# Performance work log

Hardware: AMD Instinct MI355X
Metric: run time of the kernel (lower is better)

## Reference

```python
import jax, jax.numpy as jnp
import numpy as np

V, E, T_MAX, H, L = 20000, 384, 512, 8, 8
D = E // H  # head size 48
FF = 4 * E


def setup_inputs() -> dict:
    key = jax.random.key(0)
    ks = jax.random.split(key, 24)
    B, T = 16, 512
    s = 0.02
    return {
        "index": jax.random.randint(ks[0], (B, T), 0, V, dtype=jnp.int64),
        "targets": jax.random.randint(ks[1], (B, T), 0, V, dtype=jnp.int64),
        "tok_emb": s * jax.random.normal(ks[2], (V, E), jnp.float32),
        "pos_emb": s * jax.random.normal(ks[3], (T_MAX, E), jnp.float32),
        "Wq": s * jax.random.normal(ks[4], (L, E, H, D), jnp.float32),
        "bq": jnp.zeros((L, H, D), jnp.float32),
        "Wk": s * jax.random.normal(ks[5], (L, E, H, D), jnp.float32),
        "bk": jnp.zeros((L, H, D), jnp.float32),
        "Wv": s * jax.random.normal(ks[6], (L, E, H, D), jnp.float32),
        "bv": jnp.zeros((L, H, D), jnp.float32),
        "Wo": s * jax.random.normal(ks[7], (L, E, E), jnp.float32),
        "bo": jnp.zeros((L, E), jnp.float32),
        "ln1_g": jnp.ones((L, E), jnp.float32),
        "ln1_b": jnp.zeros((L, E), jnp.float32),
        "ln2_g": jnp.ones((L, E), jnp.float32),
        "ln2_b": jnp.zeros((L, E), jnp.float32),
        "W1": s * jax.random.normal(ks[8], (L, E, FF), jnp.float32),
        "b1": jnp.zeros((L, FF), jnp.float32),
        "W2": s * jax.random.normal(ks[9], (L, FF, E), jnp.float32),
        "b2": jnp.zeros((L, E), jnp.float32),
        "lnf_g": jnp.ones((E,), jnp.float32),
        "lnf_b": jnp.zeros((E,), jnp.float32),
        "lm_b": jnp.zeros((V,), jnp.float32),
    }


def layernorm(x, g, b, eps=1e-5):
    mu = jnp.mean(x, axis=-1, keepdims=True)
    var = jnp.var(x, axis=-1, keepdims=True)
    return (x - mu) * jax.lax.rsqrt(var + eps) * g + b


def reference(index, targets, tok_emb, pos_emb, Wq, bq, Wk, bk, Wv, bv, Wo, bo,
              ln1_g, ln1_b, ln2_g, ln2_b, W1, b1, W2, b2, lnf_g, lnf_b, lm_b):
    B, T = index.shape
    x = tok_emb[index] + pos_emb[:T]  # [B,T,E]
    causal = jnp.tril(jnp.ones((T, T), bool))
    scale = D ** -0.5
    for l in range(L):
        h = layernorm(x, ln1_g[l], ln1_b[l])
        q = jnp.einsum('bte,ehd->bthd', h, Wq[l]) + bq[l]
        k = jnp.einsum('bte,ehd->bthd', h, Wk[l]) + bk[l]
        v = jnp.einsum('bte,ehd->bthd', h, Wv[l]) + bv[l]
        scores = jnp.einsum('bqhd,bkhd->bhqk', q, k) * scale
        scores = jnp.where(causal, scores, -jnp.inf)
        w = jax.nn.softmax(scores, axis=-1)
        attn = jnp.einsum('bhqk,bkhd->bqhd', w, v).reshape(B, T, E)
        x = x + attn @ Wo[l] + bo[l]
        h2 = layernorm(x, ln2_g[l], ln2_b[l])
        ff = jax.nn.gelu(h2 @ W1[l] + b1[l], approximate=False) @ W2[l] + b2[l]
        x = x + ff
    x = layernorm(x, lnf_g, lnf_b)
    logits = x @ tok_emb.T + lm_b  # tied weights
    logits = logits.reshape(B * T, V)
    logp = jax.nn.log_softmax(logits, axis=-1)
    loss = -jnp.mean(jnp.take_along_axis(logp, targets.reshape(-1, 1), axis=-1))
    return logits, loss
```

## Files before the change

### kernel.cpp

```cpp
#include <hip/hip_runtime.h>
#include <hip/hip_bf16.h>
#include <math.h>

#define M_ROWS 8192
#define E_DIM 384
#define FF_DIM 1536
#define V_DIM 20000
#define VPAD 20096
#define N_LAYER 8
#define QK_SCALE 0.14433756729740643f
#define PSTRIDE 320

typedef __bf16 bf16x8 __attribute__((ext_vector_type(8)));
typedef short  s16x8  __attribute__((ext_vector_type(8)));
typedef float  f32x4  __attribute__((ext_vector_type(4)));
typedef __hip_bfloat16 bf16_t;

__device__ __forceinline__ void gl2lds16(const void* g, void* l) {
    __builtin_amdgcn_global_load_lds((const __attribute__((address_space(1))) void*)g,
                                     (__attribute__((address_space(3))) void*)l, 16, 0, 0);
}

__global__ __launch_bounds__(256) void tconv_kernel(
    const float* __restrict__ in, bf16_t* __restrict__ out,
    int K, int N, int outRows, int rowoff)
{
    __shared__ float tile[32][33];
    const int n0 = blockIdx.x * 32, k0 = blockIdx.y * 32;
    const float* ip = in + (size_t)blockIdx.z * K * N;
    bf16_t* op = out + (size_t)blockIdx.z * outRows * K;
    const int tx = threadIdx.x & 31, ty = threadIdx.x >> 5;
#pragma unroll
    for (int i = 0; i < 32; i += 8)
        tile[ty + i][tx] = ip[(size_t)(k0 + ty + i) * N + n0 + tx];
    __syncthreads();
#pragma unroll
    for (int i = 0; i < 32; i += 8)
        op[(size_t)(rowoff + n0 + ty + i) * K + k0 + tx] = __float2bfloat16(tile[tx][ty + i]);
}

__global__ __launch_bounds__(256) void tokconv_kernel(
    const float* __restrict__ tok, bf16_t* __restrict__ out)
{
    const size_t total = (size_t)VPAD * E_DIM;
    for (size_t i = blockIdx.x * 256ull + threadIdx.x; i < total; i += gridDim.x * 256ull) {
        int row = (int)(i / E_DIM);
        int col = (int)(i - (size_t)row * E_DIM);
        float v = (row < V_DIM) ? tok[(size_t)row * E_DIM + col] : 0.f;
        out[i] = __float2bfloat16(v);
    }
}

__global__ __launch_bounds__(256) void bqkv_kernel(
    const float* __restrict__ bq, const float* __restrict__ bk,
    const float* __restrict__ bv, float* __restrict__ o)
{
    int i = blockIdx.x * 256 + threadIdx.x;
    if (i < N_LAYER * 1152) {
        int l = i / 1152, c = i - l * 1152;
        float v = (c < 384) ? bq[l * 384 + c] : (c < 768) ? bk[l * 384 + c - 384] : bv[l * 384 + c - 768];
        o[i] = v;
    }
}

__global__ __launch_bounds__(256) void embed_kernel(
    const int* __restrict__ idx, const float* __restrict__ tok,
    const float* __restrict__ pos, float* __restrict__ x)
{
    int row = blockIdx.x * 4 + (threadIdx.x >> 6);
    int lane = threadIdx.x & 63;
    int t = row & 511;
    int id = idx[row];
    const float* tr = tok + (size_t)id * E_DIM;
    const float* pr = pos + (size_t)t * E_DIM;
    float* xr = x + (size_t)row * E_DIM;
#pragma unroll
    for (int i = 0; i < 6; i++) { int c = lane + i * 64; xr[c] = tr[c] + pr[c]; }
}

__global__ __launch_bounds__(256) void ln_kernel(
    const float* __restrict__ x, const float* __restrict__ g,
    const float* __restrict__ b, bf16_t* __restrict__ out)
{
    int row = blockIdx.x * 4 + (threadIdx.x >> 6);
    int lane = threadIdx.x & 63;
    const float* xr = x + (size_t)row * E_DIM;
    float vals[6];
    float s = 0.f;
#pragma unroll
    for (int i = 0; i < 6; i++) { vals[i] = xr[lane + i * 64]; s += vals[i]; }
#pragma unroll
    for (int off = 1; off < 64; off <<= 1) s += __shfl_xor(s, off);
    float mu = s * (1.f / E_DIM);
    float sq = 0.f;
#pragma unroll
    for (int i = 0; i < 6; i++) { float d = vals[i] - mu; sq += d * d; }
#pragma unroll
    for (int off = 1; off < 64; off <<= 1) sq += __shfl_xor(sq, off);
    float rstd = rsqrtf(sq * (1.f / E_DIM) + 1e-5f);
    bf16_t* orow = out + (size_t)row * E_DIM;
#pragma unroll
    for (int i = 0; i < 6; i++) {
        int c = lane + i * 64;
        orow[c] = __float2bfloat16((vals[i] - mu) * rstd * g[c] + b[c]);
    }
}

template <int MODE, int MREP>
__global__ __launch_bounds__(256) void gemm_kernel(
    const bf16_t* __restrict__ A, const bf16_t* __restrict__ Bt,
    const float* __restrict__ bias, void* __restrict__ Cv, void* __restrict__ C2,
    int Ncols, int K)
{
    constexpr int BMR = MREP * 32;
    __shared__ __align__(16) short smem[8192];
    const int t = threadIdx.x;
    const int w = t >> 6, lane = t & 63;
    const int wm = w >> 1, wn = w & 1;
    const int bm = (MODE == 3 ? blockIdx.x : blockIdx.y) * BMR;
    const int bn = (MODE == 3 ? blockIdx.y : blockIdx.x) * 128;

    f32x4 acc[MREP][4];
#pragma unroll
    for (int m = 0; m < MREP; m++)
#pragma unroll
        for (int n = 0; n < 4; n++)
            acc[m][n] = (f32x4){0.f, 0.f, 0.f, 0.f};

    const int lg = lane >> 4;
    const int ll = lane & 15;

    for (int kt = 0; kt < K; kt += 32) {
        __syncthreads();
#pragma unroll
        for (int i = 0; i < MREP / 2; i++) {
            int li = i * 256 + t;
            int g = li >> (MREP == 4 ? 7 : 6);
            int row = li & (BMR - 1);
            gl2lds16(A + (size_t)(bm + row) * K + kt + g * 8,
                     smem + (size_t)(i * 256 + w * 64) * 8);
        }
#pragma unroll
        for (int i = 0; i < 2; i++) {
            gl2lds16(Bt + (size_t)(bn + ((i * 256 + t) & 127)) * K + kt + ((i * 256 + t) >> 7) * 8,
                     smem + 4096 + (size_t)(i * 256 + w * 64) * 8);
        }
        asm volatile("s_waitcnt vmcnt(0)" ::: "memory");
        __syncthreads();

        bf16x8 af[MREP], bfr[4];
#pragma unroll
        for (int m = 0; m < MREP; m++)
            af[m] = __builtin_bit_cast(bf16x8,
                *(const s16x8*)&smem[(lg * BMR + wm * (BMR / 2) + m * 16 + ll) * 8]);
#pragma unroll
        for (int n = 0; n < 4; n++)
            bfr[n] = __builtin_bit_cast(bf16x8,
                *(const s16x8*)&smem[4096 + (lg * 128 + wn * 64 + n * 16 + ll) * 8]);
#pragma unroll
        for (int m = 0; m < MREP; m++)
#pragma unroll
            for (int n = 0; n < 4; n++)
                acc[m][n] = __builtin_amdgcn_mfma_f32_16x16x32_bf16(af[m], bfr[n], acc[m][n], 0, 0, 0);
    }

    const int r0 = bm + wm * (BMR / 2) + (lane >> 4) * 4;
    const int c0 = bn + wn * 64 + (lane & 15);

    if (MODE == 4) {
        bf16_t* qkvb = (bf16_t*)Cv;
        bf16_t* vtb  = (bf16_t*)C2;
        const int rgn = bn / 384;
#pragma unroll
        for (int n = 0; n < 4; n++) {
            int col = c0 + n * 16;
            float bv = bias[col];
            if (rgn < 2) {
                const float sc = (rgn == 0) ? QK_SCALE : 1.f;
#pragma unroll
                for (int m = 0; m < MREP; m++) {
#pragma unroll
                    for (int j = 0; j < 4; j++) {
                        int row = r0 + m * 16 + j;
                        qkvb[(size_t)row * 1152 + col] = __float2bfloat16((acc[m][n][j] + bv) * sc);
                    }
                }
            } else {
                int cc = col - 768;
                int hh = cc / 48, dd = cc - hh * 48;
#pragma unroll
                for (int m = 0; m < MREP; m++) {
                    int row0 = r0 + m * 16;
                    int bb = row0 >> 9, tt = row0 & 511;
                    ushort4 pk;
                    pk.x = __builtin_bit_cast(unsigned short, __float2bfloat16(acc[m][n][0] + bv));
                    pk.y = __builtin_bit_cast(unsigned short, __float2bfloat16(acc[m][n][1] + bv));
                    pk.z = __builtin_bit_cast(unsigned short, __float2bfloat16(acc[m][n][2] + bv));
                    pk.w = __builtin_bit_cast(unsigned short, __float2bfloat16(acc[m][n][3] + bv));
                    *(ushort4*)&vtb[((size_t)(bb * 8 + hh) * 48 + dd) * 512 + tt] = pk;
                }
            }
        }
        return;
    }

    if (MODE == 3) {
        float* C = (float*)Cv;
        float* pbuf = (float*)C2;
        const int ptile = blockIdx.y * 2 + wn;
        float bvv[4];
#pragma unroll
        for (int n = 0; n < 4; n++) {
            int col = c0 + n * 16;
            bvv[n] = (col < Ncols) ? bias[col] : 0.f;
        }
#pragma unroll
        for (int m = 0; m < MREP; m++) {
#pragma unroll
            for (int j = 0; j < 4; j++) {
                int row = r0 + m * 16 + j;
                float se = 0.f;
#pragma unroll
                for (int n = 0; n < 4; n++) {
                    int col = c0 + n * 16;
                    if (col < Ncols) {
                        float v = acc[m][n][j] + bvv[n];
                        C[(size_t)row * Ncols + col] = v;
                        se += __expf(v);
                    }
                }
                se += __shfl_xor(se, 1);
                se += __shfl_xor(se, 2);
                se += __shfl_xor(se, 4);
                se += __shfl_xor(se, 8);
                if (ll == 0) pbuf[(size_t)row * PSTRIDE + ptile] = se;
            }
        }
        return;
    }

#pragma unroll
    for (int n = 0; n < 4; n++) {
        int col = c0 + n * 16;
        float bv = bias[col];
#pragma unroll
        for (int m = 0; m < MREP; m++) {
#pragma unroll
            for (int j = 0; j < 4; j++) {
                int row = r0 + m * 16 + j;
                float v = acc[m][n][j] + bv;
                if (MODE == 1) {
                    float* C = (float*)Cv;
                    C[(size_t)row * Ncols + col] += v;
                } else {
                    v = 0.5f * v * (1.f + erff(v * 0.70710678118654752f));
                    ((bf16_t*)Cv)[(size_t)row * Ncols + col] = __float2bfloat16(v);
                }
            }
        }
    }
}

__global__ __launch_bounds__(256) void attn_kernel(
    const bf16_t* __restrict__ qkvb, const bf16_t* __restrict__ vt,
    bf16_t* __restrict__ o)
{
    const int qt = blockIdx.x, bh = blockIdx.y;
    const int b = bh >> 3, h = bh & 7;
    __shared__ unsigned short psm[4608];
    const int tid = threadIdx.x;
    const int w = tid >> 6, lane = tid & 63;
    const int ll = lane & 15, g = lane >> 4;
    const int q0 = qt * 64;
    const int q_abs = q0 + ll * 4 + w;

    const bf16_t* qrow = qkvb + (size_t)(b * 512 + q_abs) * 1152 + h * 48;
    bf16x8 qf0 = __builtin_bit_cast(bf16x8, *(const s16x8*)(qrow + g * 8));
    bf16x8 qf1 = {};
    if (g < 2) qf1 = __builtin_bit_cast(bf16x8, *(const s16x8*)(qrow + 32 + g * 8));

    f32x4 oacc[3];
#pragma unroll
    for (int df = 0; df < 3; df++) oacc[df] = (f32x4){0.f, 0.f, 0.f, 0.f};
    float mrun = -1e30f, ssum = 0.f;

    const bf16_t* kb0 = qkvb + (size_t)b * 512 * 1152 + 384 + h * 48;
    const bf16_t* vb0 = vt + (size_t)bh * 48 * 512;
    const int ntiles = 2 * (qt + 1);

    for (int kt = 0; kt < ntiles; kt++) {
        const int kbase = kt * 32;
        f32x4 sfr[2];
#pragma unroll
        for (int f = 0; f < 2; f++) {
            const bf16_t* krow = kb0 + (size_t)(kbase + f * 16 + ll) * 1152;
            bf16x8 k0 = __builtin_bit_cast(bf16x8, *(const s16x8*)(krow + g * 8));
            bf16x8 k1 = {};
            if (g < 2) k1 = __builtin_bit_cast(bf16x8, *(const s16x8*)(krow + 32 + g * 8));
            f32x4 z = {0.f, 0.f, 0.f, 0.f};
            z = __builtin_amdgcn_mfma_f32_16x16x32_bf16(k0, qf0, z, 0, 0, 0);
            z = __builtin_amdgcn_mfma_f32_16x16x32_bf16(k1, qf1, z, 0, 0, 0);
            sfr[f] = z;
        }
        bf16x8 vf[3];
#pragma unroll
        for (int df = 0; df < 3; df++)
            vf[df] = __builtin_bit_cast(bf16x8,
                *(const s16x8*)(vb0 + (size_t)(df * 16 + ll) * 512 + kbase + g * 8));

        float p[8];
        float tmax = -1e30f;
#pragma unroll
        for (int f = 0; f < 2; f++)
#pragma unroll
            for (int j = 0; j < 4; j++) {
                int key = kbase + f * 16 + g * 4 + j;
                float sv = sfr[f][j];
                sv = (key > q_abs) ? -1e30f : sv;
                p[f * 4 + j] = sv;
                tmax = fmaxf(tmax, sv);
            }
        tmax = fmaxf(tmax, __shfl_xor(tmax, 16));
        tmax = fmaxf(tmax, __shfl_xor(tmax, 32));
        float mnew = fmaxf(mrun, tmax);
        float corr = __expf(mrun - mnew);
        float psum = 0.f;
#pragma unroll
        for (int i = 0; i < 8; i++) { p[i] = __expf(p[i] - mnew); psum += p[i]; }
        psum += __shfl_xor(psum, 16);
        psum += __shfl_xor(psum, 32);
        ssum = ssum * corr + psum;
        mrun = mnew;
#pragma unroll
        for (int df = 0; df < 3; df++)
#pragma unroll
            for (int j = 0; j < 4; j++) oacc[df][j] *= corr;

        const int pbase = (w * 2 + (kt & 1)) * 576;
#pragma unroll
        for (int f = 0; f < 2; f++)
#pragma unroll
            for (int j = 0; j < 4; j++)
                psm[pbase + (f * 16 + g * 4 + j) * 18 + ll] =
                    __builtin_bit_cast(unsigned short, __float2bfloat16(p[f * 4 + j]));
        s16x8 pr;
#pragma unroll
        for (int i = 0; i < 8; i++)
            pr[i] = (short)psm[pbase + (g * 8 + i) * 18 + ll];
        bf16x8 pf = __builtin_bit_cast(bf16x8, pr);
#pragma unroll
        for (int df = 0; df < 3; df++)
            oacc[df] = __builtin_amdgcn_mfma_f32_16x16x32_bf16(vf[df], pf, oacc[df], 0, 0, 0);
    }

    float inv = 1.f / ssum;
    bf16_t* orow = o + (size_t)(b * 512 + q_abs) * 384 + h * 48;
#pragma unroll
    for (int df = 0; df < 3; df++) {
        ushort4 pk;
        pk.x = __builtin_bit_cast(unsigned short, __float2bfloat16(oacc[df][0] * inv));
        pk.y = __builtin_bit_cast(unsigned short, __float2bfloat16(oacc[df][1] * inv));
        pk.z = __builtin_bit_cast(unsigned short, __float2bfloat16(oacc[df][2] * inv));
        pk.w = __builtin_bit_cast(unsigned short, __float2bfloat16(oacc[df][3] * inv));
        *(ushort4*)&orow[df * 16 + g * 4] = pk;
    }
}

__global__ __launch_bounds__(256) void loss_row2_kernel(
    const float* __restrict__ pbuf, const float* __restrict__ logits,
    const int* __restrict__ targets, float* __restrict__ rowloss)
{
    int row = blockIdx.x * 4 + (threadIdx.x >> 6);
    int lane = threadIdx.x & 63;
    const float* pr = pbuf + (size_t)row * PSTRIDE;
    float s = 0.f;
    for (int i = lane; i < 314; i += 64) s += pr[i];
#pragma unroll
    for (int off = 1; off < 64; off <<= 1) s += __shfl_xor(s, off);
    if (lane == 0) {
        int tgt = targets[row];
        rowloss[row] = logf(s) - logits[(size_t)row * V_DIM + tgt];
    }
}

__global__ __launch_bounds__(256) void loss_reduce_kernel(
    const float* __restrict__ rowloss, float* __restrict__ out)
{
    int t = threadIdx.x;
    __shared__ float red[4];
    float s = 0.f;
    for (int i = t; i < M_ROWS; i += 256) s += rowloss[i];
#pragma unroll
    for (int off = 1; off < 64; off <<= 1) s += __shfl_xor(s, off);
    if ((t & 63) == 0) red[t >> 6] = s;
    __syncthreads();
    if (t == 0) out[0] = (red[0] + red[1] + red[2] + red[3]) * (1.f / M_ROWS);
}

extern "C" void kernel_launch(void* const* d_in, const int* in_sizes, int n_in,
                              void* d_out, int out_size, void* d_ws, size_t ws_size,
                              hipStream_t stream)
{
    const int*   index   = (const int*)d_in[0];
    const int*   targets = (const int*)d_in[1];
    const float* tok_emb = (const float*)d_in[2];
    const float* pos_emb = (const float*)d_in[3];
    const float* Wq = (const float*)d_in[4];
    const float* bq = (const float*)d_in[5];
    const float* Wk = (const float*)d_in[6];
    const float* bk = (const float*)d_in[7];
    const float* Wv = (const float*)d_in[8];
    const float* bv = (const float*)d_in[9];
    const float* Wo = (const float*)d_in[10];
    const float* bo = (const float*)d_in[11];
    const float* ln1_g = (const float*)d_in[12];
    const float* ln1_b = (const float*)d_in[13];
    const float* ln2_g = (const float*)d_in[14];
    const float* ln2_b = (const float*)d_in[15];
    const float* W1 = (const float*)d_in[16];
    const float* b1 = (const float*)d_in[17];
    const float* W2 = (const float*)d_in[18];
    const float* b2 = (const float*)d_in[19];
    const float* lnf_g = (const float*)d_in[20];
    const float* lnf_b = (const float*)d_in[21];
    const float* lm_b  = (const float*)d_in[22];

    float* out = (float*)d_out;
    char* wsb = (char*)d_ws;

    float*  x     = (float*)(wsb + 0);
    bf16_t* hbuf  = (bf16_t*)(wsb + 12582912);
    bf16_t* obuf  = (bf16_t*)(wsb + 18874368);
    bf16_t* qkvb  = (bf16_t*)(wsb + 25165824);
    bf16_t* vtb   = (bf16_t*)(wsb + 44040192);
    bf16_t* ffmid = (bf16_t*)(wsb + 18874368);
    bf16_t* tokb  = (bf16_t*)(wsb + 50331648);
    bf16_t* qkvw  = (bf16_t*)(wsb + 65765376);
    bf16_t* wo_t  = (bf16_t*)(wsb + 72843264);
    bf16_t* w1_t  = (bf16_t*)(wsb + 75202560);
    bf16_t* w2_t  = (bf16_t*)(wsb + 84639744);
    float*  bqkv  = (float*)(wsb + 94076928);
    float*  rowloss = (float*)(wsb + 94113792);
    float*  pbuf  = (float*)(wsb + 94146560);

    tokconv_kernel<<<2048, 256, 0, stream>>>(tok_emb, tokb);
    tconv_kernel<<<dim3(12, 12, 8), 256, 0, stream>>>(Wq, qkvw, 384, 384, 1152, 0);
    tconv_kernel<<<dim3(12, 12, 8), 256, 0, stream>>>(Wk, qkvw, 384, 384, 1152, 384);
    tconv_kernel<<<dim3(12, 12, 8), 256, 0, stream>>>(Wv, qkvw, 384, 384, 1152, 768);
    tconv_kernel<<<dim3(12, 12, 8), 256, 0, stream>>>(Wo, wo_t, 384, 384, 384, 0);
    tconv_kernel<<<dim3(48, 12, 8), 256, 0, stream>>>(W1, w1_t, 384, 1536, 1536, 0);
    tconv_kernel<<<dim3(12, 48, 8), 256, 0, stream>>>(W2, w2_t, 1536, 384, 384, 0);
    bqkv_kernel<<<36, 256, 0, stream>>>(bq, bk, bv, bqkv);

    embed_kernel<<<2048, 256, 0, stream>>>(index, tok_emb, pos_emb, x);

    for (int l = 0; l < N_LAYER; l++) {
        ln_kernel<<<2048, 256, 0, stream>>>(x, ln1_g + l * E_DIM, ln1_b + l * E_DIM, hbuf);
        gemm_kernel<4, 4><<<dim3(9, 64), 256, 0, stream>>>(
            hbuf, qkvw + (size_t)l * 1152 * 384, bqkv + l * 1152, qkvb, vtb, 1152, 384);
        attn_kernel<<<dim3(8, 128), 256, 0, stream>>>(qkvb, vtb, obuf);
        gemm_kernel<1, 2><<<dim3(3, 128), 256, 0, stream>>>(
            obuf, wo_t + (size_t)l * 384 * 384, bo + l * E_DIM, x, nullptr, 384, 384);
        ln_kernel<<<2048, 256, 0, stream>>>(x, ln2_g + l * E_DIM, ln2_b + l * E_DIM, hbuf);
        gemm_kernel<2, 4><<<dim3(12, 64), 256, 0, stream>>>(
            hbuf, w1_t + (size_t)l * 1536 * 384, b1 + l * FF_DIM, ffmid, nullptr, 1536, 384);
        gemm_kernel<1, 2><<<dim3(3, 128), 256, 0, stream>>>(
            ffmid, w2_t + (size_t)l * 384 * 1536, b2 + l * E_DIM, x, nullptr, 384, 1536);
    }

    ln_kernel<<<2048, 256, 0, stream>>>(x, lnf_g, lnf_b, hbuf);
    gemm_kernel<3, 4><<<dim3(64, 157), 256, 0, stream>>>(
        hbuf, tokb, lm_b, out, pbuf, V_DIM, 384);

    loss_row2_kernel<<<2048, 256, 0, stream>>>(pbuf, out, targets, rowloss);
    loss_reduce_kernel<<<1, 256, 0, stream>>>(rowloss, out + (size_t)M_ROWS * V_DIM);
}
```

Baseline: 2.021 ms.

## Double-buffer GEMM LDS tiles to overlap global loads with MFMA

The GEMM kernel's shared-memory staging becomes a two-buffer ping-pong. Each iteration issues the next K-tile's global-to-LDS loads, then waits only for the current tile with a partial vmcnt before the MFMAs, so load latency overlaps compute. This doubles LDS use to 32 KB per block, which may lower occupancy. Correctness depends on vmcnt(NLD) matching the number of loads issued per stage.

```diff
diff --git a/kernel.cpp b/kernel.cpp
--- a/kernel.cpp
+++ b/kernel.cpp
@@ -113,7 +113,8 @@
     int Ncols, int K)
 {
     constexpr int BMR = MREP * 32;
-    __shared__ __align__(16) short smem[8192];
+    constexpr int NLD = MREP / 2 + 2;
+    __shared__ __align__(16) short smem[16384];
     const int t = threadIdx.x;
     const int w = t >> 6, lane = t & 63;
     const int wm = w >> 1, wn = w & 1;
@@ -129,39 +130,55 @@
 
     const int lg = lane >> 4;
     const int ll = lane & 15;
-
-    for (int kt = 0; kt < K; kt += 32) {
-        __syncthreads();
+    const int nt = K / 32;
+
+    auto stagef = [&](int kt, int buf) {
+        short* sA = smem + buf * 8192;
+        short* sB = sA + 4096;
 #pragma unroll
         for (int i = 0; i < MREP / 2; i++) {
             int li = i * 256 + t;
             int g = li >> (MREP == 4 ? 7 : 6);
             int row = li & (BMR - 1);
             gl2lds16(A + (size_t)(bm + row) * K + kt + g * 8,
-                     smem + (size_t)(i * 256 + w * 64) * 8);
+                     sA + (size_t)(i * 256 + w * 64) * 8);
         }
 #pragma unroll
         for (int i = 0; i < 2; i++) {
-            gl2lds16(Bt + (size_t)(bn + ((i * 256 + t) & 127)) * K + kt + ((i * 256 + t) >> 7) * 8,
-                     smem + 4096 + (size_t)(i * 256 + w * 64) * 8);
-        }
-        asm volatile("s_waitcnt vmcnt(0)" ::: "memory");
-        __syncthreads();
-
+            int li = i * 256 + t;
+            gl2lds16(Bt + (size_t)(bn + (li & 127)) * K + kt + (li >> 7) * 8,
+                     sB + (size_t)(i * 256 + w * 64) * 8);
+        }
+    };
+
+    stagef(0, 0);
+    for (int tt = 0; tt < nt; ++tt) {
+        const int buf = tt & 1;
+        if (tt + 1 < nt) {
+            stagef((tt + 1) * 32, buf ^ 1);
+            asm volatile("s_waitcnt vmcnt(%0)" :: "n"(NLD) : "memory");
+        } else {
+            asm volatile("s_waitcnt vmcnt(0)" ::: "memory");
+        }
+        __builtin_amdgcn_s_barrier();
+
+        const short* sA = smem + buf * 8192;
+        const short* sB = sA + 4096;
         bf16x8 af[MREP], bfr[4];
 #pragma unroll
         for (int m = 0; m < MREP; m++)
             af[m] = __builtin_bit_cast(bf16x8,
-                *(const s16x8*)&smem[(lg * BMR + wm * (BMR / 2) + m * 16 + ll) * 8]);
+                *(const s16x8*)&sA[(lg * BMR + wm * (BMR / 2) + m * 16 + ll) * 8]);
 #pragma unroll
         for (int n = 0; n < 4; n++)
             bfr[n] = __builtin_bit_cast(bf16x8,
-                *(const s16x8*)&smem[4096 + (lg * 128 + wn * 64 + n * 16 + ll) * 8]);
+                *(const s16x8*)&sB[(lg * 128 + wn * 64 + n * 16 + ll) * 8]);
 #pragma unroll
         for (int m = 0; m < MREP; m++)
 #pragma unroll
             for (int n = 0; n < 4; n++)
                 acc[m][n] = __builtin_amdgcn_mfma_f32_16x16x32_bf16(af[m], bfr[n], acc[m][n], 0, 0, 0);
+        __builtin_amdgcn_s_barrier();
     }
 
     const int r0 = bm + wm * (BMR / 2) + (lane >> 4) * 4;
@@ -191,13 +208,13 @@
 #pragma unroll
                 for (int m = 0; m < MREP; m++) {
                     int row0 = r0 + m * 16;
-                    int bb = row0 >> 9, tt = row0 & 511;
+                    int bb = row0 >> 9, tt2 = row0 & 511;
                     ushort4 pk;
                     pk.x = __builtin_bit_cast(unsigned short, __float2bfloat16(acc[m][n][0] + bv));
                     pk.y = __builtin_bit_cast(unsigned short, __float2bfloat16(acc[m][n][1] + bv));
                     pk.z = __builtin_bit_cast(unsigned short, __float2bfloat16(acc[m][n][2] + bv));
                     pk.w = __builtin_bit_cast(unsigned short, __float2bfloat16(acc[m][n][3] + bv));
-                    *(ushort4*)&vtb[((size_t)(bb * 8 + hh) * 48 + dd) * 512 + tt] = pk;
+                    *(ushort4*)&vtb[((size_t)(bb * 8 + hh) * 48 + dd) * 512 + tt2] = pk;
                 }
             }
         }
```

After: 2.036 ms. No clear change (+0.8%).

## Swap MFMA operands so GEMM epilogues write vectorized row-contiguous outputs

Applied to the files above, without the earlier changes.

Adds a SWAP template flag that swaps the A/B operands of the MFMA, so each lane holds four consecutive output columns of one row. The epilogues for QK projection, Wo/W2 residual add, GELU FFN and LM head can then use float4 bias loads and packed 4-wide stores instead of scalar strided stores. The QKV GEMM is split into a swapped Q/K launch and a separate non-swapped V launch that keeps the transposed V layout. This targets uncoalesced epilogue store traffic, notably the large logits write, at the cost of one extra kernel launch per layer and re-reading hbuf for V.

```diff
diff --git a/kernel.cpp b/kernel.cpp
--- a/kernel.cpp
+++ b/kernel.cpp
@@ -20,6 +20,9 @@
     __builtin_amdgcn_global_load_lds((const __attribute__((address_space(1))) void*)g,
                                      (__attribute__((address_space(3))) void*)l, 16, 0, 0);
 }
+__device__ __forceinline__ unsigned short bf16bits(float v) {
+    return __builtin_bit_cast(unsigned short, __float2bfloat16(v));
+}
 
 __global__ __launch_bounds__(256) void tconv_kernel(
     const float* __restrict__ in, bf16_t* __restrict__ out,
@@ -106,7 +109,7 @@
     }
 }
 
-template <int MODE, int MREP>
+template <int MODE, int MREP, bool SWAP>
 __global__ __launch_bounds__(256) void gemm_kernel(
     const bf16_t* __restrict__ A, const bf16_t* __restrict__ Bt,
     const float* __restrict__ bias, void* __restrict__ Cv, void* __restrict__ C2,
@@ -142,7 +145,8 @@
         }
 #pragma unroll
         for (int i = 0; i < 2; i++) {
-            gl2lds16(Bt + (size_t)(bn + ((i * 256 + t) & 127)) * K + kt + ((i * 256 + t) >> 7) * 8,
+            int li = i * 256 + t;
+            gl2lds16(Bt + (size_t)(bn + (li & 127)) * K + kt + (li >> 7) * 8,
                      smem + 4096 + (size_t)(i * 256 + w * 64) * 8);
         }
         asm volatile("s_waitcnt vmcnt(0)" ::: "memory");
@@ -160,102 +164,133 @@
 #pragma unroll
         for (int m = 0; m < MREP; m++)
 #pragma unroll
-            for (int n = 0; n < 4; n++)
-                acc[m][n] = __builtin_amdgcn_mfma_f32_16x16x32_bf16(af[m], bfr[n], acc[m][n], 0, 0, 0);
-    }
-
-    const int r0 = bm + wm * (BMR / 2) + (lane >> 4) * 4;
-    const int c0 = bn + wn * 64 + (lane & 15);
-
-    if (MODE == 4) {
-        bf16_t* qkvb = (bf16_t*)Cv;
-        bf16_t* vtb  = (bf16_t*)C2;
-        const int rgn = bn / 384;
-#pragma unroll
-        for (int n = 0; n < 4; n++) {
-            int col = c0 + n * 16;
-            float bv = bias[col];
-            if (rgn < 2) {
-                const float sc = (rgn == 0) ? QK_SCALE : 1.f;
+            for (int n = 0; n < 4; n++) {
+                if (SWAP)
+                    acc[m][n] = __builtin_amdgcn_mfma_f32_16x16x32_bf16(bfr[n], af[m], acc[m][n], 0, 0, 0);
+                else
+                    acc[m][n] = __builtin_amdgcn_mfma_f32_16x16x32_bf16(af[m], bfr[n], acc[m][n], 0, 0, 0);
+            }
+    }
+
+    if constexpr (SWAP) {
+        const int rowm0 = bm + wm * (BMR / 2) + ll;
+        const int coln0 = bn + wn * 64 + lg * 4;
+
+        if constexpr (MODE == 4) {
+            bf16_t* qkvb = (bf16_t*)Cv;
+            const float sc = (bn >= 384) ? 1.f : QK_SCALE;
+#pragma unroll
+            for (int n = 0; n < 4; n++) {
+                const int coln = coln0 + n * 16;
+                const float4 b4 = *(const float4*)&bias[coln];
 #pragma unroll
                 for (int m = 0; m < MREP; m++) {
-#pragma unroll
-                    for (int j = 0; j < 4; j++) {
-                        int row = r0 + m * 16 + j;
-                        qkvb[(size_t)row * 1152 + col] = __float2bfloat16((acc[m][n][j] + bv) * sc);
+                    const int row = rowm0 + m * 16;
+                    ushort4 pk;
+                    pk.x = bf16bits((acc[m][n][0] + b4.x) * sc);
+                    pk.y = bf16bits((acc[m][n][1] + b4.y) * sc);
+                    pk.z = bf16bits((acc[m][n][2] + b4.z) * sc);
+                    pk.w = bf16bits((acc[m][n][3] + b4.w) * sc);
+                    *(ushort4*)&qkvb[(size_t)row * 1152 + coln] = pk;
+                }
+            }
+        } else if constexpr (MODE == 1) {
+            float* C = (float*)Cv;
+#pragma unroll
+            for (int n = 0; n < 4; n++) {
+                const int coln = coln0 + n * 16;
+                const float4 b4 = *(const float4*)&bias[coln];
+#pragma unroll
+                for (int m = 0; m < MREP; m++) {
+                    const int row = rowm0 + m * 16;
+                    float4 cv = *(float4*)&C[(size_t)row * Ncols + coln];
+                    cv.x += acc[m][n][0] + b4.x;
+                    cv.y += acc[m][n][1] + b4.y;
+                    cv.z += acc[m][n][2] + b4.z;
+                    cv.w += acc[m][n][3] + b4.w;
+                    *(float4*)&C[(size_t)row * Ncols + coln] = cv;
+                }
+            }
+        } else if constexpr (MODE == 2) {
+            bf16_t* O = (bf16_t*)Cv;
+#pragma unroll
+            for (int n = 0; n < 4; n++) {
+                const int coln = coln0 + n * 16;
+                const float4 b4 = *(const float4*)&bias[coln];
+#pragma unroll
+                for (int m = 0; m < MREP; m++) {
+                    const int row = rowm0 + m * 16;
+                    float v0 = acc[m][n][0] + b4.x, v1 = acc[m][n][1] + b4.y;
+                    float v2 = acc[m][n][2] + b4.z, v3 = acc[m][n][3] + b4.w;
+                    v0 = 0.5f * v0 * (1.f + erff(v0 * 0.70710678118654752f));
+                    v1 = 0.5f * v1 * (1.f + erff(v1 * 0.70710678118654752f));
+                    v2 = 0.5f * v2 * (1.f + erff(v2 * 0.70710678118654752f));
+                    v3 = 0.5f * v3 * (1.f + erff(v3 * 0.70710678118654752f));
+                    ushort4 pk;
+                    pk.x = bf16bits(v0); pk.y = bf16bits(v1);
+                    pk.z = bf16bits(v2); pk.w = bf16bits(v3);
+                    *(ushort4*)&O[(size_t)row * Ncols + coln] = pk;
+                }
+            }
+        } else if constexpr (MODE == 3) {
+            float* C = (float*)Cv;
+            float* pbuf = (float*)C2;
+            const int ptile = blockIdx.y * 2 + wn;
+#pragma unroll
+            for (int m = 0; m < MREP; m++) {
+                const int row = rowm0 + m * 16;
+                float se = 0.f;
+#pragma unroll
+                for (int n = 0; n < 4; n++) {
+                    const int coln = coln0 + n * 16;
+                    if (coln + 3 < Ncols) {
+                        const float4 b4 = *(const float4*)&bias[coln];
+                        float4 v;
+                        v.x = acc[m][n][0] + b4.x;
+                        v.y = acc[m][n][1] + b4.y;
+                        v.z = acc[m][n][2] + b4.z;
+                        v.w = acc[m][n][3] + b4.w;
+                        *(float4*)&C[(size_t)row * Ncols + coln] = v;
+                        se += __expf(v.x) + __expf(v.y) + __expf(v.z) + __expf(v.w);
+                    } else {
+#pragma unroll
+                        for (int e = 0; e < 4; e++) {
+                            int col = coln + e;
+                            if (col < Ncols) {
+                                float v = acc[m][n][e] + bias[col];
+                                C[(size_t)row * Ncols + col] = v;
+                                se += __expf(v);
+                            }
+                        }
                     }
                 }
-            } else {
-                int cc = col - 768;
-                int hh = cc / 48, dd = cc - hh * 48;
-#pragma unroll
-                for (int m = 0; m < MREP; m++) {
-                    int row0 = r0 + m * 16;
-                    int bb = row0 >> 9, tt = row0 & 511;
-                    ushort4 pk;
-                    pk.x = __builtin_bit_cast(unsigned short, __float2bfloat16(acc[m][n][0] + bv));
-                    pk.y = __builtin_bit_cast(unsigned short, __float2bfloat16(acc[m][n][1] + bv));
-                    pk.z = __builtin_bit_cast(unsigned short, __float2bfloat16(acc[m][n][2] + bv));
-                    pk.w = __builtin_bit_cast(unsigned short, __float2bfloat16(acc[m][n][3] + bv));
-                    *(ushort4*)&vtb[((size_t)(bb * 8 + hh) * 48 + dd) * 512 + tt] = pk;
-                }
+                se += __shfl_xor(se, 16);
+                se += __shfl_xor(se, 32);
+                if (lg == 0) pbuf[(size_t)row * PSTRIDE + ptile] = se;
             }
         }
         return;
     }
 
-    if (MODE == 3) {
-        float* C = (float*)Cv;
-        float* pbuf = (float*)C2;
-        const int ptile = blockIdx.y * 2 + wn;
-        float bvv[4];
+    {
+        const int r0 = bm + wm * (BMR / 2) + lg * 4;
+        const int c0 = bn + wn * 64 + ll;
+        bf16_t* vtb = (bf16_t*)C2;
 #pragma unroll
         for (int n = 0; n < 4; n++) {
-            int col = c0 + n * 16;
-            bvv[n] = (col < Ncols) ? bias[col] : 0.f;
-        }
-#pragma unroll
-        for (int m = 0; m < MREP; m++) {
-#pragma unroll
-            for (int j = 0; j < 4; j++) {
-                int row = r0 + m * 16 + j;
-                float se = 0.f;
-#pragma unroll
-                for (int n = 0; n < 4; n++) {
-                    int col = c0 + n * 16;
-                    if (col < Ncols) {
-                        float v = acc[m][n][j] + bvv[n];
-                        C[(size_t)row * Ncols + col] = v;
-                        se += __expf(v);
-                    }
-                }
-                se += __shfl_xor(se, 1);
-                se += __shfl_xor(se, 2);
-                se += __shfl_xor(se, 4);
-                se += __shfl_xor(se, 8);
-                if (ll == 0) pbuf[(size_t)row * PSTRIDE + ptile] = se;
-            }
-        }
-        return;
-    }
-
-#pragma unroll
-    for (int n = 0; n < 4; n++) {
-        int col = c0 + n * 16;
-        float bv = bias[col];
-#pragma unroll
-        for (int m = 0; m < MREP; m++) {
-#pragma unroll
-            for (int j = 0; j < 4; j++) {
-                int row = r0 + m * 16 + j;
-                float v = acc[m][n][j] + bv;
-                if (MODE == 1) {
-                    float* C = (float*)Cv;
-                    C[(size_t)row * Ncols + col] += v;
-                } else {
-                    v = 0.5f * v * (1.f + erff(v * 0.70710678118654752f));
-                    ((bf16_t*)Cv)[(size_t)row * Ncols + col] = __float2bfloat16(v);
-                }
+            const int col = c0 + n * 16;
+            const float bv = bias[col];
+            const int hh = col / 48, dd = col - hh * 48;
+#pragma unroll
+            for (int m = 0; m < MREP; m++) {
+                const int row0 = r0 + m * 16;
+                const int bb = row0 >> 9, tt2 = row0 & 511;
+                ushort4 pk;
+                pk.x = bf16bits(acc[m][n][0] + bv);
+                pk.y = bf16bits(acc[m][n][1] + bv);
+                pk.z = bf16bits(acc[m][n][2] + bv);
+                pk.w = bf16bits(acc[m][n][3] + bv);
+                *(ushort4*)&vtb[((size_t)(bb * 8 + hh) * 48 + dd) * 512 + tt2] = pk;
             }
         }
     }
@@ -358,10 +393,10 @@
 #pragma unroll
     for (int df = 0; df < 3; df++) {
         ushort4 pk;
-        pk.x = __builtin_bit_cast(unsigned short, __float2bfloat16(oacc[df][0] * inv));
-        pk.y = __builtin_bit_cast(unsigned short, __float2bfloat16(oacc[df][1] * inv));
-        pk.z = __builtin_bit_cast(unsigned short, __float2bfloat16(oacc[df][2] * inv));
-        pk.w = __builtin_bit_cast(unsigned short, __float2bfloat16(oacc[df][3] * inv));
+        pk.x = bf16bits(oacc[df][0] * inv);
+        pk.y = bf16bits(oacc[df][1] * inv);
+        pk.z = bf16bits(oacc[df][2] * inv);
+        pk.w = bf16bits(oacc[df][3] * inv);
         *(ushort4*)&orow[df * 16 + g * 4] = pk;
     }
 }
@@ -455,21 +490,25 @@
     embed_kernel<<<2048, 256, 0, stream>>>(index, tok_emb, pos_emb, x);
 
     for (int l = 0; l < N_LAYER; l++) {
+        const bf16_t* qkvw_l = qkvw + (size_t)l * 1152 * 384;
+        const float*  bqkv_l = bqkv + l * 1152;
         ln_kernel<<<2048, 256, 0, stream>>>(x, ln1_g + l * E_DIM, ln1_b + l * E_DIM, hbuf);
-        gemm_kernel<4, 4><<<dim3(9, 64), 256, 0, stream>>>(
-            hbuf, qkvw + (size_t)l * 1152 * 384, bqkv + l * 1152, qkvb, vtb, 1152, 384);
+        gemm_kernel<4, 4, true><<<dim3(6, 64), 256, 0, stream>>>(
+            hbuf, qkvw_l, bqkv_l, qkvb, nullptr, 1152, 384);
+        gemm_kernel<5, 4, false><<<dim3(3, 64), 256, 0, stream>>>(
+            hbuf, qkvw_l + (size_t)768 * 384, bqkv_l + 768, nullptr, vtb, 384, 384);
         attn_kernel<<<dim3(8, 128), 256, 0, stream>>>(qkvb, vtb, obuf);
-        gemm_kernel<1, 2><<<dim3(3, 128), 256, 0, stream>>>(
+        gemm_kernel<1, 2, true><<<dim3(3, 128), 256, 0, stream>>>(
             obuf, wo_t + (size_t)l * 384 * 384, bo + l * E_DIM, x, nullptr, 384, 384);
         ln_kernel<<<2048, 256, 0, stream>>>(x, ln2_g + l * E_DIM, ln2_b + l * E_DIM, hbuf);
-        gemm_kernel<2, 4><<<dim3(12, 64), 256, 0, stream>>>(
+        gemm_kernel<2, 4, true><<<dim3(12, 64), 256, 0, stream>>>(
             hbuf, w1_t + (size_t)l * 1536 * 384, b1 + l * FF_DIM, ffmid, nullptr, 1536, 384);
-        gemm_kernel<1, 2><<<dim3(3, 128), 256, 0, stream>>>(
+        gemm_kernel<1, 2, true><<<dim3(3, 128), 256, 0, stream>>>(
             ffmid, w2_t + (size_t)l * 384 * 1536, b2 + l * E_DIM, x, nullptr, 384, 1536);
     }
 
     ln_kernel<<<2048, 256, 0, stream>>>(x, lnf_g, lnf_b, hbuf);
-    gemm_kernel<3, 4><<<dim3(64, 157), 256, 0, stream>>>(
+    gemm_kernel<3, 4, true><<<dim3(64, 157), 256, 0, stream>>>(
         hbuf, tokb, lm_b, out, pbuf, V_DIM, 384);
 
     loss_row2_kernel<<<2048, 256, 0, stream>>>(pbuf, out, targets, rowloss);
```

Result: no change. 1.995 ms (-1.3%).
